# Optimization experiments

Measured on AMD Instinct MI355X. Metric: run time of the kernel, lower is better.

## Reference

```python
import jax, jax.numpy as jnp
import numpy as np
from jax import lax

D_MODEL = 512
D_FIBER = 32
D_CONTROL = 64
MOMENTUM = 0.9


def setup_inputs() -> dict:
    key = jax.random.key(0)
    ks = jax.random.split(key, 7)
    B, S = 8, 4096
    hidden = jax.random.normal(ks[0], (B, S, D_MODEL), dtype=jnp.float32)
    # fiber_proj: Linear(d_model -> d_fiber)
    w_fiber = jax.random.normal(ks[1], (D_MODEL, D_FIBER), dtype=jnp.float32) / np.sqrt(D_MODEL)
    b_fiber = jnp.zeros((D_FIBER,), dtype=jnp.float32)
    # predictor: Linear(d_model+d_fiber -> d_control), GELU, Linear(d_control -> 1), Softplus
    w1 = jax.random.normal(ks[2], (D_MODEL + D_FIBER, D_CONTROL), dtype=jnp.float32) / np.sqrt(D_MODEL + D_FIBER)
    b1 = jnp.zeros((D_CONTROL,), dtype=jnp.float32)
    # nn.init.normal_(weight, std=0.01), zero bias for the last linear
    w2 = 0.01 * jax.random.normal(ks[3], (D_CONTROL, 1), dtype=jnp.float32)
    b2 = jnp.zeros((1,), dtype=jnp.float32)
    lambda_gate = jnp.asarray(1.0, dtype=jnp.float32)
    return {"hidden": hidden, "w_fiber": w_fiber, "b_fiber": b_fiber,
            "w1": w1, "b1": b1, "w2": w2, "b2": b2, "lambda_gate": lambda_gate}


def _ema_scan(delta_h, momentum):
    # field_t = momentum * field_{t-1} + (1-momentum) * delta_h_t, field_{-1}=0.
    # Same math as the original full-length causal conv1d (Toeplitz) form,
    # computed in O(S log S) via an associative scan.
    a = jnp.full_like(delta_h, momentum)
    b = (1.0 - momentum) * delta_h

    def combine(c1, c2):
        a1, b1 = c1
        a2, b2 = c2
        return (a1 * a2, a2 * b1 + b2)

    _, field = lax.associative_scan(combine, (a, b), axis=1)
    return field


def reference(hidden, w_fiber, b_fiber, w1, b1, w2, b2, lambda_gate):
    # hidden: [B, S, D]
    fiber = hidden @ w_fiber + b_fiber                      # [B, S, d_fiber]
    combined = jnp.concatenate([hidden, fiber], axis=-1)    # [B, S, D+d_fiber]
    h = jax.nn.gelu(combined @ w1 + b1, approximate=False)  # [B, S, d_control]
    delta_h = jax.nn.softplus((h @ w2 + b2).squeeze(-1))    # [B, S]
    delta_h = jnp.clip(delta_h, 0.0, 1.0)
    field = _ema_scan(delta_h, MOMENTUM)                    # [B, S]
    field = jnp.clip(field, 0.0, 10.0)
    gate = jax.nn.sigmoid(-lambda_gate * field)             # [B, S]
    return (gate, field, delta_h, fiber)
```

## Files before the change

kernel.cpp:

```cpp
#include <hip/hip_runtime.h>
#include <hip/hip_bf16.h>


#define NTOK  32768
#define SEQ   4096
#define DM    512
#define NC    96
#define TB    64
#define KC    128
#define LROW  136

typedef short bf16x8 __attribute__((ext_vector_type(8)));
typedef float f32x4  __attribute__((ext_vector_type(4)));

__device__ __forceinline__ unsigned short f2bf(float f) {
    __hip_bfloat16 h = __float2bfloat16(f);
    return *reinterpret_cast<unsigned short*>(&h);
}

__global__ __launch_bounds__(256)
void prep_kernel(const float* __restrict__ wf,
                 const float* __restrict__ bfb,
                 const float* __restrict__ w1,
                 const float* __restrict__ b1,
                 unsigned short* __restrict__ Wt,
                 float* __restrict__ bc)
{
    int idx = blockIdx.x * 256 + threadIdx.x;
    if (idx < NC * DM) {
        int n = idx >> 9, k = idx & 511;
        float v;
        if (n < 32) {
            v = wf[k * 32 + n];
        } else {
            int c = n - 32;
            v = w1[k * 64 + c];
            for (int f = 0; f < 32; ++f)
                v = fmaf(wf[k * 32 + f], w1[(512 + f) * 64 + c], v);
        }
        Wt[idx] = f2bf(v);
    }
    if (idx < NC) {
        float v;
        if (idx < 32) {
            v = bfb[idx];
        } else {
            int c = idx - 32;
            v = b1[c];
            for (int f = 0; f < 32; ++f)
                v = fmaf(bfb[f], w1[(512 + f) * 64 + c], v);
        }
        bc[idx] = v;
    }
}

__global__ __launch_bounds__(256, 2)
void fused_gemm_kernel(const float* __restrict__ hidden,
                       const unsigned short* __restrict__ Wt,
                       const float* __restrict__ bc,
                       const float* __restrict__ w2,
                       const float* __restrict__ b2,
                       float* __restrict__ out_delta,
                       float* __restrict__ out_fiber)
{
    __shared__ unsigned short a_lds[TB * LROW];
    __shared__ unsigned short b_lds[NC * LROW];

    const int tid  = threadIdx.x;
    const int wave = tid >> 6;
    const int lane = tid & 63;
    const int quad = lane >> 4;
    const int l15  = lane & 15;
    const int tok0 = blockIdx.x * TB;

    f32x4 acc[6];
#pragma unroll
    for (int t = 0; t < 6; ++t) acc[t] = (f32x4){0.f, 0.f, 0.f, 0.f};

    for (int kc = 0; kc < DM; kc += KC) {
#pragma unroll
        for (int it = 0; it < 8; ++it) {
            int v   = it * 256 + tid;
            int row = v >> 5;
            int c4  = v & 31;
            float4 u = *(const float4*)(hidden + (size_t)(tok0 + row) * DM + kc + c4 * 4);
            ushort4 o;
            o.x = f2bf(u.x); o.y = f2bf(u.y); o.z = f2bf(u.z); o.w = f2bf(u.w);
            *(ushort4*)&a_lds[row * LROW + c4 * 4] = o;
        }
#pragma unroll
        for (int it = 0; it < 6; ++it) {
            int v   = it * 256 + tid;
            int row = v >> 4;
            int c8  = v & 15;
            bf16x8 u = *(const bf16x8*)(Wt + row * DM + kc + c8 * 8);
            *(bf16x8*)&b_lds[row * LROW + c8 * 8] = u;
        }
        __syncthreads();

#pragma unroll
        for (int ks = 0; ks < 4; ++ks) {
            bf16x8 af = *(const bf16x8*)&a_lds[(wave * 16 + l15) * LROW + ks * 32 + quad * 8];
#pragma unroll
            for (int t = 0; t < 6; ++t) {
                bf16x8 bfv = *(const bf16x8*)&b_lds[(t * 16 + l15) * LROW + ks * 32 + quad * 8];
                acc[t] = __builtin_amdgcn_mfma_f32_16x16x32_bf16(af, bfv, acc[t], 0, 0, 0);
            }
        }
        __syncthreads();
    }

    const int mbase = tok0 + wave * 16 + quad * 4;

#pragma unroll
    for (int t = 0; t < 2; ++t) {
        int col = t * 16 + l15;
        float bias = bc[col];
#pragma unroll
        for (int r = 0; r < 4; ++r)
            out_fiber[(size_t)(mbase + r) * 32 + col] = acc[t][r] + bias;
    }

    float p0 = 0.f, p1 = 0.f, p2 = 0.f, p3 = 0.f;
#pragma unroll
    for (int t = 2; t < 6; ++t) {
        int c = (t - 2) * 16 + l15;
        float bias = bc[32 + c];
        float w2v  = w2[c];
        float x, g;
        x = acc[t][0] + bias; g = 0.5f * x * (1.f + erff(x * 0.70710678118f)); p0 = fmaf(g, w2v, p0);
        x = acc[t][1] + bias; g = 0.5f * x * (1.f + erff(x * 0.70710678118f)); p1 = fmaf(g, w2v, p1);
        x = acc[t][2] + bias; g = 0.5f * x * (1.f + erff(x * 0.70710678118f)); p2 = fmaf(g, w2v, p2);
        x = acc[t][3] + bias; g = 0.5f * x * (1.f + erff(x * 0.70710678118f)); p3 = fmaf(g, w2v, p3);
    }
#pragma unroll
    for (int m = 1; m <= 8; m <<= 1) {
        p0 += __shfl_xor(p0, m);
        p1 += __shfl_xor(p1, m);
        p2 += __shfl_xor(p2, m);
        p3 += __shfl_xor(p3, m);
    }
    if (l15 < 4) {
        float pv = (l15 == 0) ? p0 : (l15 == 1) ? p1 : (l15 == 2) ? p2 : p3;
        float s = pv + b2[0];
        float d = (s > 0.f) ? s + log1pf(expf(-s)) : log1pf(expf(s));
        d = fminf(fmaxf(d, 0.f), 1.f);
        out_delta[mbase + l15] = d;
    }
}

__global__ __launch_bounds__(256)
void scan_kernel(const float* __restrict__ delta,
                 const float* __restrict__ lam,
                 float* __restrict__ out_gate,
                 float* __restrict__ out_field)
{
    __shared__ float lds_d[512];
    const int b     = blockIdx.x >> 4;
    const int chunk = blockIdx.x & 15;
    const int s0    = chunk * 256;
    const int tid   = threadIdx.x;

    for (int v = tid; v < 512; v += 256) {
        int s = s0 - 256 + v;
        lds_d[v] = (s >= 0) ? delta[b * SEQ + s] : 0.f;
    }
    __syncthreads();

    float w = 0.1f, acc = 0.f;
    const int base = 256 + tid;
    for (int j = 0; j < 256; ++j) {
        acc = fmaf(w, lds_d[base - j], acc);
        w *= 0.9f;
    }
    float field = fminf(fmaxf(acc, 0.f), 10.f);

    float gate = 1.f / (1.f + expf(lam[0] * field));
    int t = b * SEQ + s0 + tid;
    out_field[t] = field;
    out_gate[t]  = gate;
}

extern "C" void kernel_launch(void* const* d_in, const int* in_sizes, int n_in,
                              void* d_out, int out_size, void* d_ws, size_t ws_size,
                              hipStream_t stream)
{
    const float* hidden = (const float*)d_in[0];
    const float* wf     = (const float*)d_in[1];
    const float* bfb    = (const float*)d_in[2];
    const float* w1     = (const float*)d_in[3];
    const float* b1     = (const float*)d_in[4];
    const float* w2     = (const float*)d_in[5];
    const float* b2     = (const float*)d_in[6];
    const float* lam    = (const float*)d_in[7];
    float* out = (float*)d_out;
    float* out_gate  = out;
    float* out_field = out + NTOK;
    float* out_delta = out + 2 * NTOK;
    float* out_fiber = out + 3 * NTOK;

    unsigned short* Wt = (unsigned short*)d_ws;
    float* bc          = (float*)((char*)d_ws + NC * DM * 2);

    hipLaunchKernelGGL(prep_kernel, dim3((NC * DM + 255) / 256), dim3(256), 0, stream,
                       wf, bfb, w1, b1, Wt, bc);
    hipLaunchKernelGGL(fused_gemm_kernel, dim3(NTOK / TB), dim3(256), 0, stream,
                       hidden, Wt, bc, w2, b2, out_delta, out_fiber);
    hipLaunchKernelGGL(scan_kernel, dim3(128), dim3(256), 0, stream,
                       out_delta, lam, out_gate, out_field);
}
```

Measured before the change: 116.1 us.

## Load A fragments directly into registers and replace windowed EMA with parallel scan

The GEMM kernel now loads each wave's hidden rows straight from global memory into register-resident bf16 MFMA fragments, so the A tile no longer goes through LDS and needs no barrier for it. The scan kernel replaces the truncated 256-tap windowed convolution with an exact per-batch parallel scan: 8 elements per thread, a wave shuffle scan, then a cross-wave prefix through shared memory. This removes LDS traffic and about 256 FMAs per output, but the scan now runs only 8 blocks, and the GEMM holds many registers for 16 fragments, which may lower occupancy.

```diff
diff --git a/kernel.cpp b/kernel.cpp
--- a/kernel.cpp
+++ b/kernel.cpp
@@ -7,7 +7,6 @@
 #define DM    512
 #define NC    96
 #define TB    64
-#define KC    128
 #define LROW  136
 
 typedef short bf16x8 __attribute__((ext_vector_type(8)));
@@ -63,7 +62,6 @@
                        float* __restrict__ out_delta,
                        float* __restrict__ out_fiber)
 {
-    __shared__ unsigned short a_lds[TB * LROW];
     __shared__ unsigned short b_lds[NC * LROW];
 
     const int tid  = threadIdx.x;
@@ -73,34 +71,44 @@
     const int l15  = lane & 15;
     const int tok0 = blockIdx.x * TB;
 
+    const float* aptr = hidden + (size_t)(tok0 + wave * 16 + l15) * DM + quad * 8;
+    bf16x8 afrag[16];
+#pragma unroll
+    for (int half = 0; half < 2; ++half) {
+        float4 raw[16];
+#pragma unroll
+        for (int i = 0; i < 16; ++i)
+            raw[i] = *(const float4*)(aptr + half * 256 + (i >> 1) * 32 + (i & 1) * 4);
+#pragma unroll
+        for (int ks = 0; ks < 8; ++ks) {
+            float4 lo = raw[ks * 2], hi = raw[ks * 2 + 1];
+            bf16x8 f;
+            f[0] = (short)f2bf(lo.x); f[1] = (short)f2bf(lo.y);
+            f[2] = (short)f2bf(lo.z); f[3] = (short)f2bf(lo.w);
+            f[4] = (short)f2bf(hi.x); f[5] = (short)f2bf(hi.y);
+            f[6] = (short)f2bf(hi.z); f[7] = (short)f2bf(hi.w);
+            afrag[half * 8 + ks] = f;
+        }
+    }
+
     f32x4 acc[6];
 #pragma unroll
     for (int t = 0; t < 6; ++t) acc[t] = (f32x4){0.f, 0.f, 0.f, 0.f};
 
-    for (int kc = 0; kc < DM; kc += KC) {
-#pragma unroll
-        for (int it = 0; it < 8; ++it) {
-            int v   = it * 256 + tid;
-            int row = v >> 5;
-            int c4  = v & 31;
-            float4 u = *(const float4*)(hidden + (size_t)(tok0 + row) * DM + kc + c4 * 4);
-            ushort4 o;
-            o.x = f2bf(u.x); o.y = f2bf(u.y); o.z = f2bf(u.z); o.w = f2bf(u.w);
-            *(ushort4*)&a_lds[row * LROW + c4 * 4] = o;
-        }
+    for (int kc = 0; kc < 4; ++kc) {
 #pragma unroll
         for (int it = 0; it < 6; ++it) {
             int v   = it * 256 + tid;
             int row = v >> 4;
             int c8  = v & 15;
-            bf16x8 u = *(const bf16x8*)(Wt + row * DM + kc + c8 * 8);
-            *(bf16x8*)&b_lds[row * LROW + c8 * 8] = u;
+            *(bf16x8*)&b_lds[row * LROW + c8 * 8] =
+                *(const bf16x8*)(Wt + row * DM + kc * 128 + c8 * 8);
         }
         __syncthreads();
 
 #pragma unroll
         for (int ks = 0; ks < 4; ++ks) {
-            bf16x8 af = *(const bf16x8*)&a_lds[(wave * 16 + l15) * LROW + ks * 32 + quad * 8];
+            bf16x8 af = afrag[kc * 4 + ks];
 #pragma unroll
             for (int t = 0; t < 6; ++t) {
                 bf16x8 bfv = *(const bf16x8*)&b_lds[(t * 16 + l15) * LROW + ks * 32 + quad * 8];
@@ -149,36 +157,64 @@
     }
 }
 
-__global__ __launch_bounds__(256)
+__global__ __launch_bounds__(512)
 void scan_kernel(const float* __restrict__ delta,
                  const float* __restrict__ lam,
                  float* __restrict__ out_gate,
                  float* __restrict__ out_field)
 {
-    __shared__ float lds_d[512];
-    const int b     = blockIdx.x >> 4;
-    const int chunk = blockIdx.x & 15;
-    const int s0    = chunk * 256;
-    const int tid   = threadIdx.x;
-
-    for (int v = tid; v < 512; v += 256) {
-        int s = s0 - 256 + v;
-        lds_d[v] = (s >= 0) ? delta[b * SEQ + s] : 0.f;
-    }
+    __shared__ float sA[8], sB[8];
+    const int b    = blockIdx.x;
+    const int tid  = threadIdx.x;
+    const int lane = tid & 63;
+    const int wv   = tid >> 6;
+
+    const float* dp = delta + (size_t)b * SEQ + tid * 8;
+    float4 d0 = *(const float4*)dp;
+    float4 d1 = *(const float4*)(dp + 4);
+    float d[8] = {d0.x, d0.y, d0.z, d0.w, d1.x, d1.y, d1.z, d1.w};
+
+    float x = 0.f;
+#pragma unroll
+    for (int j = 0; j < 8; ++j) x = fmaf(0.9f, x, 0.1f * d[j]);
+    float A = 0.430467196f;
+    float B = x;
+
+#pragma unroll
+    for (int m = 1; m <= 32; m <<= 1) {
+        float Au = __shfl_up(A, m);
+        float Bu = __shfl_up(B, m);
+        if (lane >= m) { B = fmaf(A, Bu, B); A *= Au; }
+    }
+    if (lane == 63) { sA[wv] = A; sB[wv] = B; }
     __syncthreads();
 
-    float w = 0.1f, acc = 0.f;
-    const int base = 256 + tid;
-    for (int j = 0; j < 256; ++j) {
-        acc = fmaf(w, lds_d[base - j], acc);
-        w *= 0.9f;
-    }
-    float field = fminf(fmaxf(acc, 0.f), 10.f);
-
-    float gate = 1.f / (1.f + expf(lam[0] * field));
-    int t = b * SEQ + s0 + tid;
-    out_field[t] = field;
-    out_gate[t]  = gate;
+    float cA = 1.f, cB = 0.f;
+    for (int i = 0; i < wv; ++i) { cB = fmaf(sA[i], cB, sB[i]); cA *= sA[i]; }
+
+    float Ap = __shfl_up(A, 1);
+    float Bp = __shfl_up(B, 1);
+    float f0 = (lane == 0) ? cB : fmaf(Ap, cB, Bp);
+
+    const float lamv = lam[0];
+    float xx = f0;
+    float4 of0, of1, og0, og1;
+    float* ofp = &of0.x;
+    float* ogp = &og0.x;
+#pragma unroll
+    for (int j = 0; j < 8; ++j) {
+        xx = fmaf(0.9f, xx, 0.1f * d[j]);
+        float field = fminf(fmaxf(xx, 0.f), 10.f);
+        float gate  = 1.f / (1.f + expf(lamv * field));
+        if (j < 4) { (&of0.x)[j] = field; (&og0.x)[j] = gate; }
+        else       { (&of1.x)[j - 4] = field; (&og1.x)[j - 4] = gate; }
+    }
+    (void)ofp; (void)ogp; (void)cA;
+    size_t o = (size_t)b * SEQ + tid * 8;
+    *(float4*)(out_field + o)     = of0;
+    *(float4*)(out_field + o + 4) = of1;
+    *(float4*)(out_gate  + o)     = og0;
+    *(float4*)(out_gate  + o + 4) = og1;
 }
 
 extern "C" void kernel_launch(void* const* d_in, const int* in_sizes, int n_in,
@@ -206,6 +242,6 @@
                        wf, bfb, w1, b1, Wt, bc);
     hipLaunchKernelGGL(fused_gemm_kernel, dim3(NTOK / TB), dim3(256), 0, stream,
                        hidden, Wt, bc, w2, b2, out_delta, out_fiber);
-    hipLaunchKernelGGL(scan_kernel, dim3(128), dim3(256), 0, stream,
+    hipLaunchKernelGGL(scan_kernel, dim3(8), dim3(512), 0, stream,
                        out_delta, lam, out_gate, out_field);
 }
```

After: 121.1 us. 1.04x slower.

## Load GEMM operands directly from global memory into MFMA registers, dropping LDS staging

Applied to the files above, without the earlier changes.

The fused GEMM no longer stages hidden and weight tiles through shared memory with barriers. Each lane loads its own A fragment from global memory (16 float4 per half, converted to bf16 in registers) and reads B fragments straight from the global bf16 weight buffer, which is small and likely L2/L1 resident. This removes LDS traffic and __syncthreads, and the occupancy hint in launch bounds is dropped. In exchange, every wave re-reads the weights from global or cache, and the larger register footprint may lower occupancy.

```diff
diff --git a/kernel.cpp b/kernel.cpp
--- a/kernel.cpp
+++ b/kernel.cpp
@@ -7,8 +7,6 @@
 #define DM    512
 #define NC    96
 #define TB    64
-#define KC    128
-#define LROW  136
 
 typedef short bf16x8 __attribute__((ext_vector_type(8)));
 typedef float f32x4  __attribute__((ext_vector_type(4)));
@@ -54,7 +52,7 @@
     }
 }
 
-__global__ __launch_bounds__(256, 2)
+__global__ __launch_bounds__(256)
 void fused_gemm_kernel(const float* __restrict__ hidden,
                        const unsigned short* __restrict__ Wt,
                        const float* __restrict__ bc,
@@ -63,9 +61,6 @@
                        float* __restrict__ out_delta,
                        float* __restrict__ out_fiber)
 {
-    __shared__ unsigned short a_lds[TB * LROW];
-    __shared__ unsigned short b_lds[NC * LROW];
-
     const int tid  = threadIdx.x;
     const int wave = tid >> 6;
     const int lane = tid & 63;
@@ -73,41 +68,35 @@
     const int l15  = lane & 15;
     const int tok0 = blockIdx.x * TB;
 
+    const float* aptr = hidden + (size_t)(tok0 + wave * 16 + l15) * DM + quad * 8;
+    const unsigned short* wbase = Wt + l15 * DM + quad * 8;
+
     f32x4 acc[6];
 #pragma unroll
     for (int t = 0; t < 6; ++t) acc[t] = (f32x4){0.f, 0.f, 0.f, 0.f};
 
-    for (int kc = 0; kc < DM; kc += KC) {
-#pragma unroll
-        for (int it = 0; it < 8; ++it) {
-            int v   = it * 256 + tid;
-            int row = v >> 5;
-            int c4  = v & 31;
-            float4 u = *(const float4*)(hidden + (size_t)(tok0 + row) * DM + kc + c4 * 4);
-            ushort4 o;
-            o.x = f2bf(u.x); o.y = f2bf(u.y); o.z = f2bf(u.z); o.w = f2bf(u.w);
-            *(ushort4*)&a_lds[row * LROW + c4 * 4] = o;
-        }
-#pragma unroll
-        for (int it = 0; it < 6; ++it) {
-            int v   = it * 256 + tid;
-            int row = v >> 4;
-            int c8  = v & 15;
-            bf16x8 u = *(const bf16x8*)(Wt + row * DM + kc + c8 * 8);
-            *(bf16x8*)&b_lds[row * LROW + c8 * 8] = u;
-        }
-        __syncthreads();
-
-#pragma unroll
-        for (int ks = 0; ks < 4; ++ks) {
-            bf16x8 af = *(const bf16x8*)&a_lds[(wave * 16 + l15) * LROW + ks * 32 + quad * 8];
+#pragma unroll
+    for (int half = 0; half < 2; ++half) {
+        float4 raw[16];
+#pragma unroll
+        for (int i = 0; i < 16; ++i)
+            raw[i] = *(const float4*)(aptr + half * 256 + (i >> 1) * 32 + (i & 1) * 4);
+
+#pragma unroll
+        for (int j = 0; j < 8; ++j) {
+            float4 lo = raw[j * 2], hi = raw[j * 2 + 1];
+            bf16x8 af;
+            af[0] = (short)f2bf(lo.x); af[1] = (short)f2bf(lo.y);
+            af[2] = (short)f2bf(lo.z); af[3] = (short)f2bf(lo.w);
+            af[4] = (short)f2bf(hi.x); af[5] = (short)f2bf(hi.y);
+            af[6] = (short)f2bf(hi.z); af[7] = (short)f2bf(hi.w);
+            const int ks = half * 8 + j;
 #pragma unroll
             for (int t = 0; t < 6; ++t) {
-                bf16x8 bfv = *(const bf16x8*)&b_lds[(t * 16 + l15) * LROW + ks * 32 + quad * 8];
-                acc[t] = __builtin_amdgcn_mfma_f32_16x16x32_bf16(af, bfv, acc[t], 0, 0, 0);
+                bf16x8 bv = *(const bf16x8*)(wbase + t * 16 * DM + ks * 32);
+                acc[t] = __builtin_amdgcn_mfma_f32_16x16x32_bf16(af, bv, acc[t], 0, 0, 0);
             }
         }
-        __syncthreads();
     }
 
     const int mbase = tok0 + wave * 16 + quad * 4;
```

Measured after the change: 134.9 us. 1.16x slower.
